# Kernel tuning notes

Measured on AMD Instinct MI355X. Metric: run time of the kernel, lower is better.

## Reference

```python
import jax, jax.numpy as jnp
import numpy as np

B, M, K, N = 4, 2048, 4096, 4096


def setup_inputs() -> dict:
    key = jax.random.key(0)
    k1, k2, k3, k4, k5 = jax.random.split(key, 5)
    # quantized activations in [-8, 7], stored as int8 (spec dtype int32, cast here)
    x_q = jax.random.randint(k1, (B, M, K), -8, 8, dtype=jnp.int32).astype(jnp.int8)
    # per-token activation scales (B, M, 1)
    scales_x = jax.random.uniform(k2, (B, M, 1), dtype=jnp.float32, minval=0.001, maxval=0.02)
    # int8 weight (N, K) in [-8, 7] as produced by from_float
    weight = jax.random.randint(k3, (N, K), -8, 8, dtype=jnp.int32).astype(jnp.int8)
    # per-output-row weight scales (N, 1)
    weight_scales = jax.random.uniform(k4, (N, 1), dtype=jnp.float32, minval=0.001, maxval=0.02)
    bias = jax.random.normal(k5, (N,), dtype=jnp.float32) * 0.02
    return {"x_q": x_q, "scales_x": scales_x, "weight": weight,
            "weight_scales": weight_scales, "bias": bias}


def reference(x_q, scales_x, weight, weight_scales, bias):
    acc = jnp.einsum('bmk,nk->bmn', x_q, weight,
                     preferred_element_type=jnp.int32)  # (B, M, N) int32
    # sym_dequant: per-token scale * per-row weight scale, then fused bias add
    out = acc.astype(jnp.float32) * scales_x * weight_scales.reshape(1, 1, N) + bias
    return out
```

## Files before the change

### kernel.cpp

```cpp
#include <hip/hip_runtime.h>
#include <stdint.h>

#define MROWS 8192
#define K_DIM 4096
#define N_DIM 4096
#define BM 128
#define BN 128
#define BK 64

#define X_ELEMS (MROWS * K_DIM)
#define W_ELEMS (N_DIM * K_DIM)

typedef __attribute__((ext_vector_type(4))) int int4v;

#define GLOAD_LDS16(gptr, lptr)                                                   \
    __builtin_amdgcn_global_load_lds((const __attribute__((address_space(1))) void*)(gptr), \
                                     (__attribute__((address_space(3))) void*)(lptr), 16, 0, 0)

__global__ __launch_bounds__(256) void pack_i32_to_i8(
    const int4v* __restrict__ src, int* __restrict__ dst, int n4)
{
    int i = blockIdx.x * blockDim.x + threadIdx.x;
    if (i >= n4) return;
    int4v v = src[i];
    unsigned p = (unsigned)(v[0] & 0xFF)
               | ((unsigned)(v[1] & 0xFF) << 8)
               | ((unsigned)(v[2] & 0xFF) << 16)
               | ((unsigned)(v[3] & 0xFF) << 24);
    dst[i] = (int)p;
}

__global__ __launch_bounds__(256) void i8gemm_dq_kernel(
    const int8_t* __restrict__ xq,
    const float*  __restrict__ sx,
    const int8_t* __restrict__ wt,
    const float*  __restrict__ ws,
    const float*  __restrict__ bias,
    float*        __restrict__ out)
{
    __shared__ __align__(16) int8_t lsA[BM * BK];
    __shared__ __align__(16) int8_t lsB[BN * BK];

    const int tid  = threadIdx.x;
    const int wave = tid >> 6;
    const int lane = tid & 63;

    const int ct = blockIdx.x & 31;
    const int rt = blockIdx.x >> 5;

    const int wr = wave >> 1;
    const int wc = wave & 1;

    const int srow = wave * 16 + (lane >> 2);
    const int scol = (lane & 3) * 16;
    const int8_t* gA = xq + (size_t)(rt * BM + srow) * K_DIM + scol;
    const int8_t* gB = wt + (size_t)(ct * BN + srow) * K_DIM + scol;
    int8_t* lA = lsA + wave * 1024;
    int8_t* lB = lsB + wave * 1024;

    const int mrow = lane & 15;
    const int kch  = (lane >> 4) * 16;

    int4v acc[4][4] = {};

    const int kIters = K_DIM / BK;
    for (int kt = 0; kt < kIters; ++kt) {
        GLOAD_LDS16(gA,              lA);
        GLOAD_LDS16(gA + 64 * K_DIM, lA + 4096);
        GLOAD_LDS16(gB,              lB);
        GLOAD_LDS16(gB + 64 * K_DIM, lB + 4096);
        gA += BK;
        gB += BK;
        __syncthreads();

        int4v afrag[4], bfrag[4];
        #pragma unroll
        for (int i = 0; i < 4; ++i)
            afrag[i] = *(const int4v*)(lsA + (wr * 64 + i * 16 + mrow) * BK + kch);
        #pragma unroll
        for (int j = 0; j < 4; ++j)
            bfrag[j] = *(const int4v*)(lsB + (wc * 64 + j * 16 + mrow) * BK + kch);

        #pragma unroll
        for (int i = 0; i < 4; ++i)
            #pragma unroll
            for (int j = 0; j < 4; ++j)
                acc[i][j] = __builtin_amdgcn_mfma_i32_16x16x64_i8(
                                afrag[i], bfrag[j], acc[i][j], 0, 0, 0);

        __syncthreads();
    }

    const int row_base = rt * BM + wr * 64;
    const int col_base = ct * BN + wc * 64;
    const int crow = (lane >> 4) * 4;
    const int ccol = lane & 15;

    float wsc[4], bsc[4];
    #pragma unroll
    for (int j = 0; j < 4; ++j) {
        const int c = col_base + j * 16 + ccol;
        wsc[j] = ws[c];
        bsc[j] = bias[c];
    }

    #pragma unroll
    for (int i = 0; i < 4; ++i) {
        const int r0 = row_base + i * 16 + crow;
        float sx4[4];
        #pragma unroll
        for (int r = 0; r < 4; ++r) sx4[r] = sx[r0 + r];
        #pragma unroll
        for (int j = 0; j < 4; ++j) {
            const int c = col_base + j * 16 + ccol;
            float* o = out + (size_t)r0 * N_DIM + c;
            #pragma unroll
            for (int r = 0; r < 4; ++r)
                o[(size_t)r * N_DIM] = (float)acc[i][j][r] * sx4[r] * wsc[j] + bsc[j];
        }
    }
}

extern "C" void kernel_launch(void* const* d_in, const int* in_sizes, int n_in,
                              void* d_out, int out_size, void* d_ws, size_t ws_size,
                              hipStream_t stream) {
    const int*   xq32 = (const int*)d_in[0];
    const float* sx   = (const float*)d_in[1];
    const int*   wt32 = (const int*)d_in[2];
    const float* ws   = (const float*)d_in[3];
    const float* bias = (const float*)d_in[4];
    float* out = (float*)d_out;

    int8_t* xq8 = (int8_t*)d_ws;
    int8_t* wt8 = xq8 + (size_t)X_ELEMS;

    {
        int n4x = X_ELEMS / 4;
        int n4w = W_ELEMS / 4;
        pack_i32_to_i8<<<n4x / 256, 256, 0, stream>>>((const int4v*)xq32, (int*)xq8, n4x);
        pack_i32_to_i8<<<n4w / 256, 256, 0, stream>>>((const int4v*)wt32, (int*)wt8, n4w);
    }

    dim3 grid((MROWS / BM) * (N_DIM / BN));
    i8gemm_dq_kernel<<<grid, 256, 0, stream>>>(xq8, sx, wt8, ws, bias, out);
}
```

Before: 416.7 us.

## Switch to 32x32x32 int8 MFMA and widen int32-to-int8 pack kernel

Replaces the 16x16x64 int8 MFMA tiling with 32x32x32 MFMA instructions, changing fragment loads and the accumulator layout. The epilogue is rewritten for the 32x32 output register mapping. The pack kernel now processes 16 elements per thread with 16-byte stores, cutting thread count. Per-thread strided loads in the pack kernel may reduce coalescing.

Result: slower. 453.9 us (+8.9%).

```diff
diff --git a/kernel.cpp b/kernel.cpp
--- a/kernel.cpp
+++ b/kernel.cpp
@@ -11,23 +11,32 @@
 #define X_ELEMS (MROWS * K_DIM)
 #define W_ELEMS (N_DIM * K_DIM)
 
-typedef __attribute__((ext_vector_type(4))) int int4v;
+typedef __attribute__((ext_vector_type(4)))  int int4v;
+typedef __attribute__((ext_vector_type(16))) int int16v;
 
 #define GLOAD_LDS16(gptr, lptr)                                                   \
     __builtin_amdgcn_global_load_lds((const __attribute__((address_space(1))) void*)(gptr), \
                                      (__attribute__((address_space(3))) void*)(lptr), 16, 0, 0)
 
+__device__ __forceinline__ int pack4(int4v v) {
+    return (int)((unsigned)(v[0] & 0xFF)
+               | ((unsigned)(v[1] & 0xFF) << 8)
+               | ((unsigned)(v[2] & 0xFF) << 16)
+               | ((unsigned)(v[3] & 0xFF) << 24));
+}
+
 __global__ __launch_bounds__(256) void pack_i32_to_i8(
-    const int4v* __restrict__ src, int* __restrict__ dst, int n4)
+    const int4v* __restrict__ src, int4v* __restrict__ dst, int n16)
 {
     int i = blockIdx.x * blockDim.x + threadIdx.x;
-    if (i >= n4) return;
-    int4v v = src[i];
-    unsigned p = (unsigned)(v[0] & 0xFF)
-               | ((unsigned)(v[1] & 0xFF) << 8)
-               | ((unsigned)(v[2] & 0xFF) << 16)
-               | ((unsigned)(v[3] & 0xFF) << 24);
-    dst[i] = (int)p;
+    if (i >= n16) return;
+    int4v a = src[4 * i + 0];
+    int4v b = src[4 * i + 1];
+    int4v c = src[4 * i + 2];
+    int4v d = src[4 * i + 3];
+    int4v r;
+    r[0] = pack4(a); r[1] = pack4(b); r[2] = pack4(c); r[3] = pack4(d);
+    dst[i] = r;
 }
 
 __global__ __launch_bounds__(256) void i8gemm_dq_kernel(
@@ -58,10 +67,10 @@
     int8_t* lA = lsA + wave * 1024;
     int8_t* lB = lsB + wave * 1024;
 
-    const int mrow = lane & 15;
-    const int kch  = (lane >> 4) * 16;
+    const int m32   = lane & 31;
+    const int khalf = (lane >> 5) * 16;
 
-    int4v acc[4][4] = {};
+    int16v acc[2][2] = {};
 
     const int kIters = K_DIM / BK;
     for (int kt = 0; kt < kIters; ++kt) {
@@ -73,50 +82,59 @@
         gB += BK;
         __syncthreads();
 
-        int4v afrag[4], bfrag[4];
+        int4v af[2][2], bf[2][2];
         #pragma unroll
-        for (int i = 0; i < 4; ++i)
-            afrag[i] = *(const int4v*)(lsA + (wr * 64 + i * 16 + mrow) * BK + kch);
+        for (int i = 0; i < 2; ++i)
+            #pragma unroll
+            for (int s = 0; s < 2; ++s)
+                af[i][s] = *(const int4v*)(lsA + (wr * 64 + i * 32 + m32) * BK + s * 32 + khalf);
         #pragma unroll
-        for (int j = 0; j < 4; ++j)
-            bfrag[j] = *(const int4v*)(lsB + (wc * 64 + j * 16 + mrow) * BK + kch);
+        for (int j = 0; j < 2; ++j)
+            #pragma unroll
+            for (int s = 0; s < 2; ++s)
+                bf[j][s] = *(const int4v*)(lsB + (wc * 64 + j * 32 + m32) * BK + s * 32 + khalf);
 
         #pragma unroll
-        for (int i = 0; i < 4; ++i)
+        for (int s = 0; s < 2; ++s)
             #pragma unroll
-            for (int j = 0; j < 4; ++j)
-                acc[i][j] = __builtin_amdgcn_mfma_i32_16x16x64_i8(
-                                afrag[i], bfrag[j], acc[i][j], 0, 0, 0);
+            for (int i = 0; i < 2; ++i)
+                #pragma unroll
+                for (int j = 0; j < 2; ++j)
+                    acc[i][j] = __builtin_amdgcn_mfma_i32_32x32x32_i8(
+                                    af[i][s], bf[j][s], acc[i][j], 0, 0, 0);
 
         __syncthreads();
     }
 
     const int row_base = rt * BM + wr * 64;
     const int col_base = ct * BN + wc * 64;
-    const int crow = (lane >> 4) * 4;
-    const int ccol = lane & 15;
+    const int ccol  = lane & 31;
+    const int rquad = (lane >> 5) * 4;
 
-    float wsc[4], bsc[4];
+    float wsc[2], bsc[2];
     #pragma unroll
-    for (int j = 0; j < 4; ++j) {
-        const int c = col_base + j * 16 + ccol;
+    for (int j = 0; j < 2; ++j) {
+        const int c = col_base + j * 32 + ccol;
         wsc[j] = ws[c];
         bsc[j] = bias[c];
     }
 
     #pragma unroll
-    for (int i = 0; i < 4; ++i) {
-        const int r0 = row_base + i * 16 + crow;
-        float sx4[4];
+    for (int i = 0; i < 2; ++i) {
+        float sxv[16];
         #pragma unroll
-        for (int r = 0; r < 4; ++r) sx4[r] = sx[r0 + r];
+        for (int reg = 0; reg < 16; ++reg) {
+            const int r = row_base + i * 32 + (reg & 3) + 8 * (reg >> 2) + rquad;
+            sxv[reg] = sx[r];
+        }
         #pragma unroll
-        for (int j = 0; j < 4; ++j) {
-            const int c = col_base + j * 16 + ccol;
-            float* o = out + (size_t)r0 * N_DIM + c;
+        for (int j = 0; j < 2; ++j) {
+            const int c = col_base + j * 32 + ccol;
             #pragma unroll
-            for (int r = 0; r < 4; ++r)
-                o[(size_t)r * N_DIM] = (float)acc[i][j][r] * sx4[r] * wsc[j] + bsc[j];
+            for (int reg = 0; reg < 16; ++reg) {
+                const int r = row_base + i * 32 + (reg & 3) + 8 * (reg >> 2) + rquad;
+                out[(size_t)r * N_DIM + c] = (float)acc[i][j][reg] * sxv[reg] * wsc[j] + bsc[j];
+            }
         }
     }
 }
@@ -135,10 +153,10 @@
     int8_t* wt8 = xq8 + (size_t)X_ELEMS;
 
     {
-        int n4x = X_ELEMS / 4;
-        int n4w = W_ELEMS / 4;
-        pack_i32_to_i8<<<n4x / 256, 256, 0, stream>>>((const int4v*)xq32, (int*)xq8, n4x);
-        pack_i32_to_i8<<<n4w / 256, 256, 0, stream>>>((const int4v*)wt32, (int*)wt8, n4w);
+        int n16x = X_ELEMS / 16;
+        int n16w = W_ELEMS / 16;
+        pack_i32_to_i8<<<n16x / 256, 256, 0, stream>>>((const int4v*)xq32, (int4v*)xq8, n16x);
+        pack_i32_to_i8<<<n16w / 256, 256, 0, stream>>>((const int4v*)wt32, (int4v*)wt8, n16w);
     }
 
     dim3 grid((MROWS / BM) * (N_DIM / BN));
```
